# Optimization experiments

Measured on AMD Instinct MI355X. Metric: run time of the kernel, lower is better.

The kernel has to match this reference:

```python
import jax, jax.numpy as jnp
import numpy as np

H = 256   # hidden_size
IN = 2    # adding-problem input features
B, T = 128, 1024


def setup_inputs() -> dict:
    key = jax.random.key(0)
    ks = jax.random.split(key, 12)
    sc = 1.0 / np.sqrt(H)
    u = lambda k, shape: jax.random.uniform(k, shape, minval=-sc, maxval=sc, dtype=jnp.float32)
    return {
        "x": jax.random.normal(ks[0], (B, T, IN), dtype=jnp.float32),
        # GRU weights (torch layout: [3H, in], gate order r, z, n)
        "W_ih": u(ks[1], (3 * H, IN)),
        "W_hh": u(ks[2], (3 * H, H)),
        "b_ih": u(ks[3], (3 * H,)),
        "b_hh": u(ks[4], (3 * H,)),
        # adaptive momentum coefficient beta_t = sigmoid(x W + h U + b)
        "Wb_x": u(ks[5], (IN, 1)),
        "Wb_h": u(ks[6], (H, 1)),
        "b_beta": jnp.zeros((1,), dtype=jnp.float32),
        # momentum step size s (learnable scalar)
        "s": jnp.ones((), dtype=jnp.float32),
        # read-out head Linear(H, 1)
        "W_head": u(ks[7], (1, H)),
        "b_head": u(ks[8], (1,)),
    }


def reference(x, W_ih, W_hh, b_ih, b_hh, Wb_x, Wb_h, b_beta, s, W_head, b_head):
    Bm = x.shape[0]

    def step(carry, x_t):
        h, v = carry                                    # h: [B,H], v: [B,3H]
        beta = jax.nn.sigmoid(x_t @ Wb_x + h @ Wb_h + b_beta)   # [B,1]
        p = x_t @ W_ih.T + b_ih                         # input projection [B,3H]
        v = beta * v + s * p                            # momentum buffer
        gh = h @ W_hh.T + b_hh                          # hidden projection [B,3H]
        vr, vz, vn = jnp.split(v, 3, axis=-1)
        hr, hz, hn = jnp.split(gh, 3, axis=-1)
        r = jax.nn.sigmoid(vr + hr)
        z = jax.nn.sigmoid(vz + hz)
        n = jnp.tanh(vn + r * hn)
        h_new = (1.0 - z) * n + z * h
        return (h_new, v), beta[:, 0]

    h0 = jnp.zeros((Bm, H), dtype=x.dtype)
    v0 = jnp.zeros((Bm, 3 * H), dtype=x.dtype)
    (hT, _), betas = jax.lax.scan(step, (h0, v0), jnp.transpose(x, (1, 0, 2)))
    out = hT @ W_head.T + b_head                        # head on last timestep, [B,1]
    return (out, betas.T)                               # betas: [B,T]
```

## Files before the change

kernel.cpp:

```cpp
#include <hip/hip_runtime.h>

#define HID 256
#define TLEN 1024
#define BATCH 128

typedef _Float16 half2_t __attribute__((ext_vector_type(2)));

__device__ __forceinline__ float fexp2(float x) { return __builtin_amdgcn_exp2f(x); }
__device__ __forceinline__ float frcp(float x)  { return __builtin_amdgcn_rcpf(x); }
__device__ __forceinline__ float fast_sigmoid(float x) {
  return frcp(1.0f + fexp2(-1.442695040888963f * x));
}
__device__ __forceinline__ float fast_tanh(float x) {
  float e = fexp2(2.885390081777927f * x);
  return 1.0f - 2.0f * frcp(e + 1.0f);
}
__device__ __forceinline__ float dot2acc(half2_t a, half2_t b, float c) {
  return __builtin_amdgcn_fdot2(a, b, c, false);
}

#if defined(__has_builtin) && __has_builtin(__builtin_amdgcn_sdot4)
#define SDOT4(a, b, c) __builtin_amdgcn_sdot4((int)(a), (int)(b), (c), false)
#else
__device__ __forceinline__ int SDOT4(int a, int b, int c) {
#pragma unroll
  for (int e = 0; e < 4; ++e)
    c += ((a << (24 - 8 * e)) >> 24) * ((b << (24 - 8 * e)) >> 24);
  return c;
}
#endif

#define DPP_ADD_F(var, ctrl, rmask)                                            \
  var += __builtin_bit_cast(float, __builtin_amdgcn_update_dpp(                \
      0, __builtin_bit_cast(int, var), (ctrl), (rmask), 0xf, true))
#define DPP_ADD_I(var, ctrl)                                                   \
  var += __builtin_amdgcn_update_dpp(0, (var), (ctrl), 0xf, 0xf, true)
#define DPP_MOV_I(dst, src, ctrl)                                              \
  dst = __builtin_amdgcn_update_dpp(0, (src), (ctrl), 0xf, 0xf, true)

__device__ __forceinline__ float wave_sum63(float p) {
  DPP_ADD_F(p, 0x111, 0xf);
  DPP_ADD_F(p, 0x112, 0xf);
  DPP_ADD_F(p, 0x114, 0xf);
  DPP_ADD_F(p, 0x118, 0xf);
  DPP_ADD_F(p, 0x142, 0xa);
  DPP_ADD_F(p, 0x143, 0xc);
  return p;
}

__global__ void quant_whh(const float* __restrict__ W_hh, uint4* __restrict__ wq,
                          float* __restrict__ scales) {
  const int r = blockIdx.x * 256 + threadIdx.x;
  if (r >= 768) return;
  const float* row = W_hh + (size_t)r * HID;
  float amax = 0.0f;
  for (int k = 0; k < HID; ++k) amax = fmaxf(amax, fabsf(row[k]));
  amax = fmaxf(amax, 1e-20f);
  scales[r] = amax / 127.0f;
  const float inv = 127.0f / amax;
  const int g = r >> 8, d = r & 255;
  for (int half = 0; half < 2; ++half) {
    for (int j = 0; j < 8; ++j) {
      unsigned w[4];
#pragma unroll
      for (int u = 0; u < 4; ++u) {
        unsigned bb = 0;
#pragma unroll
        for (int e = 0; e < 4; ++e) {
          int qv = (int)rintf(row[128 * half + 16 * j + 4 * u + e] * inv);
          bb |= (unsigned)(qv & 0xff) << (8 * e);
        }
        w[u] = bb;
      }
      wq[(size_t)(2 * d + half) * 24 + g * 8 + j] = uint4{w[0], w[1], w[2], w[3]};
    }
  }
}

__global__ __launch_bounds__(512, 1)
void momgru_persistent(const float* __restrict__ x,
                       const float* __restrict__ W_ih,
                       const float* __restrict__ b_ih,
                       const float* __restrict__ b_hh,
                       const float* __restrict__ Wb_x,
                       const float* __restrict__ Wb_h,
                       const float* __restrict__ b_beta,
                       const float* __restrict__ s_ptr,
                       const float* __restrict__ W_head,
                       const float* __restrict__ b_head,
                       const uint4* __restrict__ wq,
                       const float* __restrict__ scales,
                       float* __restrict__ out)
{
  const int b    = blockIdx.x;
  const int tid  = threadIdx.x;
  const int lane = tid & 63;
  const int wv   = tid >> 6;
  const int d    = tid >> 1;
  const int half = tid & 1;

  __shared__ unsigned hq[2][64];
  __shared__ float    red[2][8];

  const uint4* wqt = wq + (size_t)tid * 24;
  uint4 wr[8], wz[8], wn[8];
#pragma unroll
  for (int j = 0; j < 8; ++j) wr[j] = wqt[j];
#pragma unroll
  for (int j = 0; j < 8; ++j) wz[j] = wqt[8 + j];
#pragma unroll
  for (int j = 0; j < 8; ++j) wn[j] = wqt[16 + j];

  const float sv = s_ptr[0];
  const half2_t wih_r = half2_t{(_Float16)(sv * W_ih[2 * d]),             (_Float16)(sv * W_ih[2 * d + 1])};
  const half2_t wih_z = half2_t{(_Float16)(sv * W_ih[2 * (HID + d)]),     (_Float16)(sv * W_ih[2 * (HID + d) + 1])};
  const half2_t wih_n = half2_t{(_Float16)(sv * W_ih[2 * (2 * HID + d)]), (_Float16)(sv * W_ih[2 * (2 * HID + d) + 1])};
  const float bih_r = sv * b_ih[d], bih_z = sv * b_ih[HID + d], bih_n = sv * b_ih[2 * HID + d];
  const float bhh_r = b_hh[d], bhh_z = b_hh[HID + d], bhh_n = b_hh[2 * HID + d];
  const float sc_r = scales[d] * (1.0f / 127.0f);
  const float sc_z = scales[HID + d] * (1.0f / 127.0f);
  const float sc_n = scales[2 * HID + d] * (1.0f / 127.0f);
  const half2_t wbx2 = half2_t{(_Float16)Wb_x[0], (_Float16)Wb_x[1]};
  const float bbeta = b_beta[0];
  const float wbh_t = Wb_h[d];

  if (tid < 128) reinterpret_cast<unsigned*>(hq)[tid] = 0u;
  if (tid < 16) reinterpret_cast<float*>(red)[tid] = 0.0f;
  float h_old = 0.0f, vr = 0.0f, vz = 0.0f, vn = 0.0f;
  float* betas = out + BATCH;
  const float2* xg2 = reinterpret_cast<const float2*>(x + (size_t)b * TLEN * 2);
  float2 xv = xg2[0];
  __syncthreads();

  int cur = 0;
  for (int t = 0; t < TLEN; ++t) {
    int ar = 0, az = 0, an = 0;
    const int4* hb = reinterpret_cast<const int4*>(hq[cur]);
#pragma unroll
    for (int j = 0; j < 8; ++j) {
      const int4 hv = hb[8 * half + j];
      ar = SDOT4(hv.x, wr[j].x, ar);
      az = SDOT4(hv.x, wz[j].x, az);
      an = SDOT4(hv.x, wn[j].x, an);
      ar = SDOT4(hv.y, wr[j].y, ar);
      az = SDOT4(hv.y, wz[j].y, az);
      an = SDOT4(hv.y, wn[j].y, an);
      ar = SDOT4(hv.z, wr[j].z, ar);
      az = SDOT4(hv.z, wz[j].z, az);
      an = SDOT4(hv.z, wn[j].z, an);
      ar = SDOT4(hv.w, wr[j].w, ar);
      az = SDOT4(hv.w, wz[j].w, az);
      an = SDOT4(hv.w, wn[j].w, an);
    }
    DPP_ADD_I(ar, 0xB1);
    DPP_ADD_I(az, 0xB1);
    DPP_ADD_I(an, 0xB1);

    const int rp = (t + 1) & 1;
    const float hWb = red[rp][0] + red[rp][1] + red[rp][2] + red[rp][3] +
                      red[rp][4] + red[rp][5] + red[rp][6] + red[rp][7];
    const half2_t x2 = half2_t{(_Float16)xv.x, (_Float16)xv.y};
    xv = xg2[(t + 1 < TLEN) ? t + 1 : t];
    const float beta = fast_sigmoid(dot2acc(x2, wbx2, hWb + bbeta));
    vr = beta * vr + dot2acc(x2, wih_r, bih_r);
    vz = beta * vz + dot2acc(x2, wih_z, bih_z);
    vn = beta * vn + dot2acc(x2, wih_n, bih_n);

    const float r = fast_sigmoid(vr + (float)ar * sc_r + bhh_r);
    const float z = fast_sigmoid(vz + (float)az * sc_z + bhh_z);
    const float n = fast_tanh(vn + r * ((float)an * sc_n + bhh_n));
    h_old = (1.0f - z) * n + z * h_old;

    const int nxt = cur ^ 1;
    const int qb = ((int)rintf(h_old * 127.0f)) & 0xff;
    int q2, q4, q6;
    DPP_MOV_I(q2, qb, 0x102);
    DPP_MOV_I(q4, qb, 0x104);
    DPP_MOV_I(q6, qb, 0x106);
    if ((tid & 7) == 0)
      hq[nxt][tid >> 3] = (unsigned)(qb | (q2 << 8) | (q4 << 16) | (q6 << 24));

    float p = (half == 0) ? h_old * wbh_t : 0.0f;
    p = wave_sum63(p);
    if (lane == 63) red[t & 1][wv] = p;
    if (tid == 63) betas[(size_t)b * TLEN + t] = beta;

    __syncthreads();
    cur = nxt;
  }

  float hp = (half == 0) ? h_old * W_head[d] : 0.0f;
  hp = wave_sum63(hp);
  if (lane == 63) red[0][wv] = hp;
  __syncthreads();
  if (tid == 0) {
    out[b] = red[0][0] + red[0][1] + red[0][2] + red[0][3] +
             red[0][4] + red[0][5] + red[0][6] + red[0][7] + b_head[0];
  }
}

extern "C" void kernel_launch(void* const* d_in, const int* in_sizes, int n_in,
                              void* d_out, int out_size, void* d_ws, size_t ws_size,
                              hipStream_t stream) {
  const float* x      = (const float*)d_in[0];
  const float* W_ih   = (const float*)d_in[1];
  const float* W_hh   = (const float*)d_in[2];
  const float* b_ih   = (const float*)d_in[3];
  const float* b_hh   = (const float*)d_in[4];
  const float* Wb_x   = (const float*)d_in[5];
  const float* Wb_h   = (const float*)d_in[6];
  const float* b_beta = (const float*)d_in[7];
  const float* s      = (const float*)d_in[8];
  const float* W_head = (const float*)d_in[9];
  const float* b_head = (const float*)d_in[10];
  float* out = (float*)d_out;

  uint4* wq     = (uint4*)d_ws;
  float* scales = (float*)((char*)d_ws + 512 * 24 * 16);

  quant_whh<<<dim3(3), dim3(256), 0, stream>>>(W_hh, wq, scales);
  momgru_persistent<<<dim3(BATCH), dim3(512), 0, stream>>>(
      x, W_ih, b_ih, b_hh, Wb_x, Wb_h, b_beta, s, W_head, b_head,
      (const uint4*)wq, (const float*)scales, out);
}
```

Before: 960.9 us.

## Assign one hidden unit per thread, halving block size to 256 threads

Each thread now owns a full hidden unit and computes its entire 256-length int8 dot product, so the cross-lane DPP reduction of partial sums is gone. Blocks shrink from 512 to 256 threads (4 waves), which makes the per-step barrier and the beta partial-sum reduction cheaper. The quantized weight layout is reorganized so each thread holds 48 uint4 of weights in registers. In exchange, the serial dot-product chain per thread doubles in length and register pressure rises, which may lengthen each timestep.

After: 891.0 us. 1.08x faster.

```diff
diff --git a/kernel.cpp b/kernel.cpp
--- a/kernel.cpp
+++ b/kernel.cpp
@@ -33,8 +33,6 @@
 #define DPP_ADD_F(var, ctrl, rmask)                                            \
   var += __builtin_bit_cast(float, __builtin_amdgcn_update_dpp(                \
       0, __builtin_bit_cast(int, var), (ctrl), (rmask), 0xf, true))
-#define DPP_ADD_I(var, ctrl)                                                   \
-  var += __builtin_amdgcn_update_dpp(0, (var), (ctrl), 0xf, 0xf, true)
 #define DPP_MOV_I(dst, src, ctrl)                                              \
   dst = __builtin_amdgcn_update_dpp(0, (src), (ctrl), 0xf, 0xf, true)
 
@@ -58,26 +56,24 @@
   amax = fmaxf(amax, 1e-20f);
   scales[r] = amax / 127.0f;
   const float inv = 127.0f / amax;
-  const int g = r >> 8, d = r & 255;
-  for (int half = 0; half < 2; ++half) {
-    for (int j = 0; j < 8; ++j) {
-      unsigned w[4];
-#pragma unroll
-      for (int u = 0; u < 4; ++u) {
-        unsigned bb = 0;
-#pragma unroll
-        for (int e = 0; e < 4; ++e) {
-          int qv = (int)rintf(row[128 * half + 16 * j + 4 * u + e] * inv);
-          bb |= (unsigned)(qv & 0xff) << (8 * e);
-        }
-        w[u] = bb;
+  const int g = r >> 8, dd = r & 255;
+  for (int c = 0; c < 16; ++c) {
+    unsigned w[4];
+#pragma unroll
+    for (int u = 0; u < 4; ++u) {
+      unsigned bb = 0;
+#pragma unroll
+      for (int e = 0; e < 4; ++e) {
+        int qv = (int)rintf(row[16 * c + 4 * u + e] * inv);
+        bb |= (unsigned)(qv & 0xff) << (8 * e);
       }
-      wq[(size_t)(2 * d + half) * 24 + g * 8 + j] = uint4{w[0], w[1], w[2], w[3]};
+      w[u] = bb;
     }
+    wq[(size_t)dd * 48 + g * 16 + c] = uint4{w[0], w[1], w[2], w[3]};
   }
 }
 
-__global__ __launch_bounds__(512, 1)
+__global__ __launch_bounds__(256, 1)
 void momgru_persistent(const float* __restrict__ x,
                        const float* __restrict__ W_ih,
                        const float* __restrict__ b_ih,
@@ -96,36 +92,34 @@
   const int tid  = threadIdx.x;
   const int lane = tid & 63;
   const int wv   = tid >> 6;
-  const int d    = tid >> 1;
-  const int half = tid & 1;
 
   __shared__ unsigned hq[2][64];
-  __shared__ float    red[2][8];
-
-  const uint4* wqt = wq + (size_t)tid * 24;
-  uint4 wr[8], wz[8], wn[8];
-#pragma unroll
-  for (int j = 0; j < 8; ++j) wr[j] = wqt[j];
-#pragma unroll
-  for (int j = 0; j < 8; ++j) wz[j] = wqt[8 + j];
-#pragma unroll
-  for (int j = 0; j < 8; ++j) wn[j] = wqt[16 + j];
+  __shared__ float    red[2][4];
+
+  const uint4* wqt = wq + (size_t)tid * 48;
+  uint4 wr[16], wz[16], wn[16];
+#pragma unroll
+  for (int j = 0; j < 16; ++j) wr[j] = wqt[j];
+#pragma unroll
+  for (int j = 0; j < 16; ++j) wz[j] = wqt[16 + j];
+#pragma unroll
+  for (int j = 0; j < 16; ++j) wn[j] = wqt[32 + j];
 
   const float sv = s_ptr[0];
-  const half2_t wih_r = half2_t{(_Float16)(sv * W_ih[2 * d]),             (_Float16)(sv * W_ih[2 * d + 1])};
-  const half2_t wih_z = half2_t{(_Float16)(sv * W_ih[2 * (HID + d)]),     (_Float16)(sv * W_ih[2 * (HID + d) + 1])};
-  const half2_t wih_n = half2_t{(_Float16)(sv * W_ih[2 * (2 * HID + d)]), (_Float16)(sv * W_ih[2 * (2 * HID + d) + 1])};
-  const float bih_r = sv * b_ih[d], bih_z = sv * b_ih[HID + d], bih_n = sv * b_ih[2 * HID + d];
-  const float bhh_r = b_hh[d], bhh_z = b_hh[HID + d], bhh_n = b_hh[2 * HID + d];
-  const float sc_r = scales[d] * (1.0f / 127.0f);
-  const float sc_z = scales[HID + d] * (1.0f / 127.0f);
-  const float sc_n = scales[2 * HID + d] * (1.0f / 127.0f);
+  const half2_t wih_r = half2_t{(_Float16)(sv * W_ih[2 * tid]),             (_Float16)(sv * W_ih[2 * tid + 1])};
+  const half2_t wih_z = half2_t{(_Float16)(sv * W_ih[2 * (HID + tid)]),     (_Float16)(sv * W_ih[2 * (HID + tid) + 1])};
+  const half2_t wih_n = half2_t{(_Float16)(sv * W_ih[2 * (2 * HID + tid)]), (_Float16)(sv * W_ih[2 * (2 * HID + tid) + 1])};
+  const float bih_r = sv * b_ih[tid], bih_z = sv * b_ih[HID + tid], bih_n = sv * b_ih[2 * HID + tid];
+  const float bhh_r = b_hh[tid], bhh_z = b_hh[HID + tid], bhh_n = b_hh[2 * HID + tid];
+  const float sc_r = scales[tid] * (1.0f / 127.0f);
+  const float sc_z = scales[HID + tid] * (1.0f / 127.0f);
+  const float sc_n = scales[2 * HID + tid] * (1.0f / 127.0f);
   const half2_t wbx2 = half2_t{(_Float16)Wb_x[0], (_Float16)Wb_x[1]};
   const float bbeta = b_beta[0];
-  const float wbh_t = Wb_h[d];
+  const float wbh_t = Wb_h[tid];
 
   if (tid < 128) reinterpret_cast<unsigned*>(hq)[tid] = 0u;
-  if (tid < 16) reinterpret_cast<float*>(red)[tid] = 0.0f;
+  if (tid < 8) reinterpret_cast<float*>(red)[tid] = 0.0f;
   float h_old = 0.0f, vr = 0.0f, vz = 0.0f, vn = 0.0f;
   float* betas = out + BATCH;
   const float2* xg2 = reinterpret_cast<const float2*>(x + (size_t)b * TLEN * 2);
@@ -137,28 +131,24 @@
     int ar = 0, az = 0, an = 0;
     const int4* hb = reinterpret_cast<const int4*>(hq[cur]);
 #pragma unroll
-    for (int j = 0; j < 8; ++j) {
-      const int4 hv = hb[8 * half + j];
-      ar = SDOT4(hv.x, wr[j].x, ar);
-      az = SDOT4(hv.x, wz[j].x, az);
-      an = SDOT4(hv.x, wn[j].x, an);
-      ar = SDOT4(hv.y, wr[j].y, ar);
-      az = SDOT4(hv.y, wz[j].y, az);
-      an = SDOT4(hv.y, wn[j].y, an);
-      ar = SDOT4(hv.z, wr[j].z, ar);
-      az = SDOT4(hv.z, wz[j].z, az);
-      an = SDOT4(hv.z, wn[j].z, an);
-      ar = SDOT4(hv.w, wr[j].w, ar);
-      az = SDOT4(hv.w, wz[j].w, az);
-      an = SDOT4(hv.w, wn[j].w, an);
+    for (int c = 0; c < 16; ++c) {
+      const int4 hv = hb[c];
+      ar = SDOT4(hv.x, wr[c].x, ar);
+      az = SDOT4(hv.x, wz[c].x, az);
+      an = SDOT4(hv.x, wn[c].x, an);
+      ar = SDOT4(hv.y, wr[c].y, ar);
+      az = SDOT4(hv.y, wz[c].y, az);
+      an = SDOT4(hv.y, wn[c].y, an);
+      ar = SDOT4(hv.z, wr[c].z, ar);
+      az = SDOT4(hv.z, wz[c].z, az);
+      an = SDOT4(hv.z, wn[c].z, an);
+      ar = SDOT4(hv.w, wr[c].w, ar);
+      az = SDOT4(hv.w, wz[c].w, az);
+      an = SDOT4(hv.w, wn[c].w, an);
     }
-    DPP_ADD_I(ar, 0xB1);
-    DPP_ADD_I(az, 0xB1);
-    DPP_ADD_I(an, 0xB1);
 
     const int rp = (t + 1) & 1;
-    const float hWb = red[rp][0] + red[rp][1] + red[rp][2] + red[rp][3] +
-                      red[rp][4] + red[rp][5] + red[rp][6] + red[rp][7];
+    const float hWb = red[rp][0] + red[rp][1] + red[rp][2] + red[rp][3];
     const half2_t x2 = half2_t{(_Float16)xv.x, (_Float16)xv.y};
     xv = xg2[(t + 1 < TLEN) ? t + 1 : t];
     const float beta = fast_sigmoid(dot2acc(x2, wbx2, hWb + bbeta));
@@ -173,30 +163,27 @@
 
     const int nxt = cur ^ 1;
     const int qb = ((int)rintf(h_old * 127.0f)) & 0xff;
-    int q2, q4, q6;
+    int q1, q2, q3;
+    DPP_MOV_I(q1, qb, 0x101);
     DPP_MOV_I(q2, qb, 0x102);
-    DPP_MOV_I(q4, qb, 0x104);
-    DPP_MOV_I(q6, qb, 0x106);
-    if ((tid & 7) == 0)
-      hq[nxt][tid >> 3] = (unsigned)(qb | (q2 << 8) | (q4 << 16) | (q6 << 24));
-
-    float p = (half == 0) ? h_old * wbh_t : 0.0f;
+    DPP_MOV_I(q3, qb, 0x103);
+    if ((tid & 3) == 0)
+      hq[nxt][tid >> 2] = (unsigned)(qb | (q1 << 8) | (q2 << 16) | (q3 << 24));
+
+    float p = h_old * wbh_t;
     p = wave_sum63(p);
     if (lane == 63) red[t & 1][wv] = p;
-    if (tid == 63) betas[(size_t)b * TLEN + t] = beta;
+    if (tid == 0) betas[(size_t)b * TLEN + t] = beta;
 
     __syncthreads();
     cur = nxt;
   }
 
-  float hp = (half == 0) ? h_old * W_head[d] : 0.0f;
+  float hp = h_old * W_head[tid];
   hp = wave_sum63(hp);
   if (lane == 63) red[0][wv] = hp;
   __syncthreads();
-  if (tid == 0) {
-    out[b] = red[0][0] + red[0][1] + red[0][2] + red[0][3] +
-             red[0][4] + red[0][5] + red[0][6] + red[0][7] + b_head[0];
-  }
+  if (tid == 0) out[b] = red[0][0] + red[0][1] + red[0][2] + red[0][3] + b_head[0];
 }
 
 extern "C" void kernel_launch(void* const* d_in, const int* in_sizes, int n_in,
@@ -216,10 +203,10 @@
   float* out = (float*)d_out;
 
   uint4* wq     = (uint4*)d_ws;
-  float* scales = (float*)((char*)d_ws + 512 * 24 * 16);
+  float* scales = (float*)((char*)d_ws + 256 * 48 * 16);
 
   quant_whh<<<dim3(3), dim3(256), 0, stream>>>(W_hh, wq, scales);
-  momgru_persistent<<<dim3(BATCH), dim3(512), 0, stream>>>(
+  momgru_persistent<<<dim3(BATCH), dim3(256), 0, stream>>>(
       x, W_ih, b_ih, b_hh, Wb_x, Wb_h, b_beta, s, W_head, b_head,
       (const uint4*)wq, (const float*)scales, out);
 }
```
